# Kernel optimization log

Measured on AMD Instinct MI355X. Metric: run time of the kernel, lower is better.

The kernel has to match this reference:

```python
import jax, jax.numpy as jnp
import numpy as np

NUM_HEADS = 8
HEAD_DIM = 128
ATTN_SCALE = 0.12


def _rotary_tables(T, head_dim, dtype=jnp.float32):
    # modded-nanogpt half-truncated RoPE: rotate only first half of freq slots
    quarter = head_dim // 4
    angular = (1.0 / 1024.0) ** jnp.linspace(0.0, 1.0, quarter, dtype=dtype)
    angular = jnp.concatenate([angular, jnp.zeros(quarter, dtype=dtype)])  # [head_dim//2]
    t = jnp.arange(T, dtype=dtype)
    theta = t[:, None] * angular[None, :]  # [T, head_dim//2]
    return jnp.cos(theta), jnp.sin(theta)


def _apply_rotary(x, cos, sin):
    # x: [B, T, H, D]; cos/sin: [T, D//2]
    x1, x2 = jnp.split(x, 2, axis=-1)
    c = cos[None, :, None, :]
    s = sin[None, :, None, :]
    y1 = x1 * c + x2 * s
    y2 = -x1 * s + x2 * c
    return jnp.concatenate([y1, y2], axis=-1)


def _rms_norm(x):
    eps = jnp.asarray(jnp.finfo(x.dtype).eps, x.dtype)
    var = jnp.mean(jnp.square(x), axis=-1, keepdims=True)
    return x * jax.lax.rsqrt(var + eps)


def setup_inputs() -> dict:
    key = jax.random.key(0)
    k1, k2, k3, k4, k5 = jax.random.split(key, 5)
    B, T, D = 1, 4096, 1024
    hdim = NUM_HEADS * HEAD_DIM
    std = 0.5 * D ** (-0.5)
    x = jax.random.normal(k1, (B, T, D), dtype=jnp.float32)
    ve = jax.random.normal(k2, (B, T, hdim), dtype=jnp.float32)
    qkv_w = jax.random.normal(k3, (3, hdim, D), dtype=jnp.float32) * std
    lambdas = jnp.array([0.5, 0.5], dtype=jnp.float32)
    c_proj_w = jax.random.normal(k5, (D, hdim), dtype=jnp.float32) * std
    return {"x": x, "ve": ve, "qkv_w": qkv_w, "lambdas": lambdas, "c_proj_w": c_proj_w}


def reference(x, ve, qkv_w, lambdas, c_proj_w):
    B, T, D = x.shape
    H, Hd = NUM_HEADS, HEAD_DIM
    # QKV projection: qkv_w [3, H*Hd, D]
    qkv = jnp.einsum('btd,ckd->btck', x, qkv_w)  # [B, T, 3, H*Hd]
    qkv = qkv.reshape(B, T, 3, H, Hd)
    q, k, v = qkv[:, :, 0], qkv[:, :, 1], qkv[:, :, 2]  # [B, T, H, Hd]
    # QK RMSNorm
    q = _rms_norm(q)
    k = _rms_norm(k)
    # RoPE
    cos, sin = _rotary_tables(T, Hd, dtype=x.dtype)
    q = _apply_rotary(q, cos, sin)
    k = _apply_rotary(k, cos, sin)
    # value-embedding lambda mix
    v = lambdas[0] * v + lambdas[1] * ve.reshape(B, T, H, Hd)
    # causal attention with fixed scale 0.12 (block-causal FlexAttention mask)
    scores = jnp.einsum('bthd,bshd->bhts', q, k) * ATTN_SCALE  # [B, H, T, T]
    causal = jnp.tril(jnp.ones((T, T), dtype=bool))
    scores = jnp.where(causal[None, None], scores, jnp.asarray(-jnp.inf, scores.dtype))
    probs = jax.nn.softmax(scores, axis=-1)
    y = jnp.einsum('bhts,bshd->bthd', probs, v)  # [B, T, H, Hd]
    y = y.reshape(B, T, H * Hd)
    return y @ c_proj_w.T  # [B, T, D]
```

## Files before the change

kernel.cpp:

```cpp
#include <hip/hip_runtime.h>

typedef __bf16 bf16;
typedef __bf16 bf16x8 __attribute__((ext_vector_type(8)));
typedef __bf16 bf16x4 __attribute__((ext_vector_type(4)));
typedef __bf16 bf16x2 __attribute__((ext_vector_type(2)));
typedef float f32x4 __attribute__((ext_vector_type(4)));
typedef float f32x16 __attribute__((ext_vector_type(16)));
typedef int i32x4 __attribute__((ext_vector_type(4)));
typedef int i32x2 __attribute__((ext_vector_type(2)));

#define GLL16(gp, lp)                                                          \
  __builtin_amdgcn_global_load_lds(                                            \
      (const __attribute__((address_space(1))) unsigned int*)(gp),             \
      (__attribute__((address_space(3))) unsigned int*)(lp), 16, 0, 0)

__global__ __launch_bounds__(256) void cast3_f32_bf16(
    const float* __restrict__ a, bf16* __restrict__ oa, int na4,
    const float* __restrict__ b, bf16* __restrict__ ob, int nb4,
    const float* __restrict__ c, bf16* __restrict__ oc, int nc4) {
  int i = blockIdx.x * blockDim.x + threadIdx.x;
  int stride = gridDim.x * blockDim.x;
  int total = na4 + nb4 + nc4;
  for (; i < total; i += stride) {
    const float4* src;
    bf16x4* dst;
    int j = i;
    if (j < na4) {
      src = (const float4*)a + j; dst = (bf16x4*)oa + j;
    } else if ((j -= na4) < nb4) {
      src = (const float4*)b + j; dst = (bf16x4*)ob + j;
    } else {
      j -= nb4;
      src = (const float4*)c + j; dst = (bf16x4*)oc + j;
    }
    float4 v = *src;
    bf16x4 o;
    o[0] = (bf16)v.x; o[1] = (bf16)v.y; o[2] = (bf16)v.z; o[3] = (bf16)v.w;
    *dst = o;
  }
}

template <int K, int LDC, int BM, typename CT>
__global__ __launch_bounds__(256) void gemm_bt(
    const bf16* __restrict__ A, const bf16* __restrict__ B,
    CT* __restrict__ C) {
  __shared__ __align__(16) bf16 As[BM * 64];
  __shared__ __align__(16) bf16 Bs[128 * 64];
  const int tid  = threadIdx.x;
  const int lane = tid & 63;
  const int wave = tid >> 6;
  const int ln15 = lane & 15, quad = lane >> 4;
  const int wm = wave >> 1, wn = wave & 1;
  const int m0 = blockIdx.y * BM, n0 = blockIdx.x * 128;
  constexpr int MI = BM / 32;

  f32x4 acc[MI][4] = {};

  for (int k0 = 0; k0 < K; k0 += 64) {
    __syncthreads();
#pragma unroll
    for (int j = 0; j < BM / 32; ++j) {
      int gbase = j * 256 + wave * 64;
      int g = gbase + lane;
      int r = g >> 3, c = (g & 7) ^ (r & 7);
      GLL16(A + (size_t)(m0 + r) * K + k0 + c * 8, As + (size_t)gbase * 8);
    }
#pragma unroll
    for (int j = 0; j < 4; ++j) {
      int gbase = j * 256 + wave * 64;
      int g = gbase + lane;
      int r = g >> 3, c = (g & 7) ^ (r & 7);
      GLL16(B + (size_t)(n0 + r) * K + k0 + c * 8, Bs + (size_t)gbase * 8);
    }
    __syncthreads();
#pragma unroll
    for (int kk = 0; kk < 2; ++kk) {
      bf16x8 af[MI], bfr[4];
#pragma unroll
      for (int mi = 0; mi < MI; ++mi) {
        int m = wm * (BM / 2) + mi * 16 + ln15;
        int cg = kk * 4 + quad;
        af[mi] = *(const bf16x8*)(As + (m * 8 + (cg ^ (m & 7))) * 8);
      }
#pragma unroll
      for (int ni = 0; ni < 4; ++ni) {
        int n = wn * 64 + ni * 16 + ln15;
        int cg = kk * 4 + quad;
        bfr[ni] = *(const bf16x8*)(Bs + (n * 8 + (cg ^ (n & 7))) * 8);
      }
#pragma unroll
      for (int mi = 0; mi < MI; ++mi)
#pragma unroll
        for (int ni = 0; ni < 4; ++ni)
          acc[mi][ni] = __builtin_amdgcn_mfma_f32_16x16x32_bf16(
              af[mi], bfr[ni], acc[mi][ni], 0, 0, 0);
    }
  }
#pragma unroll
  for (int mi = 0; mi < MI; ++mi)
#pragma unroll
    for (int ni = 0; ni < 4; ++ni)
#pragma unroll
      for (int r = 0; r < 4; ++r) {
        int row = m0 + wm * (BM / 2) + mi * 16 + quad * 4 + r;
        int col = n0 + wn * 64 + ni * 16 + ln15;
        C[(size_t)row * LDC + col] = (CT)acc[mi][ni][r];
      }
}

__global__ __launch_bounds__(256) void qkv_post(
    const bf16* __restrict__ qkv, const float* __restrict__ ve,
    const float* __restrict__ lambdas, bf16* __restrict__ qn,
    bf16* __restrict__ kn, bf16* __restrict__ vt) {
  const int h  = blockIdx.x;
  const int t0 = blockIdx.y * 64;
  const int tid = threadIdx.x;
  const int wave = tid >> 6, lane = tid & 63;
  __shared__ __align__(16) float tile[64][129];

  const int j = lane;
  float cth = 1.0f, sth = 0.0f;
  for (int i = 0; i < 16; ++i) {
    int t = t0 + wave * 16 + i;
    if (j < 32) {
      float ang = exp2f((float)j * (-10.0f / 31.0f));
      float th = (float)t * ang;
      __sincosf(th, &sth, &cth);
    }
#pragma unroll
    for (int qk = 0; qk < 2; ++qk) {
      const bf16* row = qkv + (size_t)t * 3072 + qk * 1024 + h * 128;
      float x1 = (float)row[j], x2 = (float)row[j + 64];
      float ss = x1 * x1 + x2 * x2;
#pragma unroll
      for (int m = 1; m < 64; m <<= 1) ss += __shfl_xor(ss, m, 64);
      float rinv = rsqrtf(ss * (1.0f / 128.0f) + 1.1920929e-7f);
      if (qk == 0) rinv *= 0.12f;
      float y1 = (x1 * cth + x2 * sth) * rinv;
      float y2 = (x2 * cth - x1 * sth) * rinv;
      bf16* orow = (qk == 0 ? qn : kn) + (size_t)t * 1024 + h * 128;
      orow[j] = (bf16)y1;
      orow[j + 64] = (bf16)y2;
    }
  }

  float l0 = lambdas[0], l1 = lambdas[1];
  for (int c = 0; c < 32; ++c) {
    int idx = c * 256 + tid;
    int d = idx & 127, tl = idx >> 7;
    int t = t0 + tl;
    float v = (float)qkv[(size_t)t * 3072 + 2048 + h * 128 + d];
    float vev = ve[(size_t)t * 1024 + h * 128 + d];
    tile[tl][d] = l0 * v + l1 * vev;
  }
  __syncthreads();
  for (int c = 0; c < 32; ++c) {
    int idx = c * 256 + tid;
    int tl = idx & 63, d = idx >> 6;
    vt[((size_t)(h * 128 + d)) * 4096 + t0 + tl] = (bf16)tile[tl][d];
  }
}

__global__ __launch_bounds__(256, 2) void flash_attn(
    const bf16* __restrict__ qn, const bf16* __restrict__ kn,
    const bf16* __restrict__ vt, float* __restrict__ Op,
    float* __restrict__ ls) {
  const int id = blockIdx.x;
  const int qt = (id < 256) ? (31 - (id >> 4)) : ((id - 256) >> 4);
  const int sub = id & 15;
  const int h = sub >> 1;
  const int half = sub & 1;
  const int tid = threadIdx.x;
  const int wave = tid >> 6, lane = tid & 63;
  const int l31 = lane & 31, hl = lane >> 5;

  __shared__ __align__(16) bf16 smem[4 * 64 * 128];
  bf16* Ks = smem;
  bf16* Vs = smem + 2 * 64 * 128;

  const int nkv = 2 * (qt + 1);
  const int half0 = qt + 1;
  const int kt_begin = half ? half0 : 0;
  const int kt_end = half ? nkv : half0;
  const int niter = kt_end - kt_begin;
  const int pidx = (h * 32 + qt) * 2 + half;

  const int qminw = qt * 128 + wave * 32;
  const int qg = qminw + l31;

  bf16x8 qf[8];
  {
    const bf16* qb = qn + (size_t)qg * 1024 + h * 128 + hl * 8;
#pragma unroll
    for (int f = 0; f < 8; ++f) qf[f] = *(const bf16x8*)(qb + f * 16);
  }

  f32x16 acc_o[4] = {};
  float rs = 0.0f;

  auto prefetch = [&](int kt, int buf) {
    const int kv0 = kt * 64;
    bf16* ks = Ks + buf * (64 * 128);
    bf16* vs = Vs + buf * (128 * 64);
#pragma unroll
    for (int jj = 0; jj < 4; ++jj) {
      int gbase = jj * 256 + wave * 64;
      int g = gbase + lane;
      int r = g >> 4, c = (g & 15) ^ (r & 15);
      GLL16(kn + (size_t)(kv0 + r) * 1024 + h * 128 + c * 8,
            ks + (size_t)gbase * 8);
    }
#pragma unroll
    for (int jj = 0; jj < 4; ++jj) {
      int gbase = jj * 256 + wave * 64;
      int g = gbase + lane;
      int d = g >> 3, c = (g & 7) ^ (d & 7);
      GLL16(vt + ((size_t)(h * 128 + d)) * 4096 + kv0 + c * 8,
            vs + (size_t)gbase * 8);
    }
  };

  prefetch(kt_begin, 0);

  for (int it = 0; it < niter; ++it) {
    const int kt = kt_begin + it;
    const int kv0 = kt * 64;
    __syncthreads();
    if (it + 1 < niter) prefetch(kt + 1, (it + 1) & 1);
    const bf16* ksb = Ks + (it & 1) * (64 * 128);
    const bf16* vsb = Vs + (it & 1) * (128 * 64);

    if (kv0 > qminw + 31) continue;

    f32x16 acc0 = {}, acc1 = {};
    const int l15 = l31 & 15;
    __builtin_amdgcn_s_setprio(1);
#pragma unroll
    for (int f = 0; f < 8; ++f) {
      bf16x8 a0 = *(const bf16x8*)(
          ksb + (l31 * 16 + ((2 * f + hl) ^ l15)) * 8);
      bf16x8 a1 = *(const bf16x8*)(
          ksb + ((32 + l31) * 16 + ((2 * f + hl) ^ l15)) * 8);
      acc0 = __builtin_amdgcn_mfma_f32_32x32x16_bf16(a0, qf[f], acc0, 0, 0, 0);
      acc1 = __builtin_amdgcn_mfma_f32_32x32x16_bf16(a1, qf[f], acc1, 0, 0, 0);
    }
    __builtin_amdgcn_s_setprio(0);

    const bool needmask = (kv0 + 63 > qminw);
    float rsp[4] = {0.f, 0.f, 0.f, 0.f};
    if (needmask) {
#pragma unroll
      for (int r = 0; r < 16; ++r) {
        int kvl = (r & 3) + 8 * (r >> 2) + 4 * hl;
        float v0 = __expf(acc0[r]);
        float v1 = __expf(acc1[r]);
        if (kv0 + kvl > qg) v0 = 0.0f;
        if (kv0 + 32 + kvl > qg) v1 = 0.0f;
        acc0[r] = v0; acc1[r] = v1;
        rsp[r & 3] += v0 + v1;
      }
    } else {
#pragma unroll
      for (int r = 0; r < 16; ++r) {
        float v0 = __expf(acc0[r]);
        float v1 = __expf(acc1[r]);
        acc0[r] = v0; acc1[r] = v1;
        rsp[r & 3] += v0 + v1;
      }
    }
    rs += (rsp[0] + rsp[1]) + (rsp[2] + rsp[3]);

    int pk0[8], pk1[8];
#pragma unroll
    for (int g = 0; g < 8; ++g) {
      bf16x2 t0, t1;
      t0[0] = (bf16)acc0[2 * g]; t0[1] = (bf16)acc0[2 * g + 1];
      t1[0] = (bf16)acc1[2 * g]; t1[1] = (bf16)acc1[2 * g + 1];
      pk0[g] = __builtin_bit_cast(int, t0);
      pk1[g] = __builtin_bit_cast(int, t1);
    }

    bf16x8 pf[4];
#if __has_builtin(__builtin_amdgcn_permlane32_swap)
#pragma unroll
    for (int cc = 0; cc < 4; ++cc) {
      int s0 = (cc < 2) ? pk0[(cc & 1) * 4 + 0] : pk1[(cc & 1) * 4 + 0];
      int s1 = (cc < 2) ? pk0[(cc & 1) * 4 + 1] : pk1[(cc & 1) * 4 + 1];
      int s2 = (cc < 2) ? pk0[(cc & 1) * 4 + 2] : pk1[(cc & 1) * 4 + 2];
      int s3 = (cc < 2) ? pk0[(cc & 1) * 4 + 3] : pk1[(cc & 1) * 4 + 3];
      i32x2 r02 = __builtin_amdgcn_permlane32_swap(s0, s2, false, false);
      i32x2 r13 = __builtin_amdgcn_permlane32_swap(s1, s3, false, false);
      i32x4 dv;
      dv[0] = r02[0];
      dv[1] = r13[0];
      dv[2] = r02[1];
      dv[3] = r13[1];
      pf[cc] = __builtin_bit_cast(bf16x8, dv);
    }
#else
#pragma unroll
    for (int cc = 0; cc < 4; ++cc) {
      int s0 = (cc < 2) ? pk0[(cc & 1) * 4 + 0] : pk1[(cc & 1) * 4 + 0];
      int s1 = (cc < 2) ? pk0[(cc & 1) * 4 + 1] : pk1[(cc & 1) * 4 + 1];
      int s2 = (cc < 2) ? pk0[(cc & 1) * 4 + 2] : pk1[(cc & 1) * 4 + 2];
      int s3 = (cc < 2) ? pk0[(cc & 1) * 4 + 3] : pk1[(cc & 1) * 4 + 3];
      int sh0 = __shfl_xor(s0, 32, 64);
      int sh1 = __shfl_xor(s1, 32, 64);
      int sh2 = __shfl_xor(s2, 32, 64);
      int sh3 = __shfl_xor(s3, 32, 64);
      int own0 = hl ? s2 : s0;
      int own1 = hl ? s3 : s1;
      int par0 = hl ? sh2 : sh0;
      int par1 = hl ? sh3 : sh1;
      i32x4 dv;
      dv[0] = hl ? par0 : own0;
      dv[1] = hl ? par1 : own1;
      dv[2] = hl ? own0 : par0;
      dv[3] = hl ? own1 : par1;
      pf[cc] = __builtin_bit_cast(bf16x8, dv);
    }
#endif

    __builtin_amdgcn_s_setprio(1);
#pragma unroll
    for (int dt = 0; dt < 4; ++dt) {
      int vrow = dt * 32 + l31;
#pragma unroll
      for (int cc = 0; cc < 4; ++cc) {
        bf16x8 a = *(const bf16x8*)(
            vsb + (vrow * 8 + ((2 * cc + hl) ^ (vrow & 7))) * 8);
        acc_o[dt] =
            __builtin_amdgcn_mfma_f32_32x32x16_bf16(a, pf[cc], acc_o[dt], 0, 0, 0);
      }
    }
    __builtin_amdgcn_s_setprio(0);
  }

  rs += __shfl_xor(rs, 32, 64);
  if (hl == 0) ls[pidx * 128 + wave * 32 + l31] = rs;
  float* opb = Op + (size_t)pidx * 16384 + (size_t)(wave * 32 + l31) * 128;
#pragma unroll
  for (int dt = 0; dt < 4; ++dt)
#pragma unroll
    for (int rg = 0; rg < 4; ++rg) {
      float4 o;
      o.x = acc_o[dt][rg * 4 + 0];
      o.y = acc_o[dt][rg * 4 + 1];
      o.z = acc_o[dt][rg * 4 + 2];
      o.w = acc_o[dt][rg * 4 + 3];
      int d0 = dt * 32 + 4 * hl + 8 * rg;
      *(float4*)(opb + d0) = o;
    }
}

__global__ __launch_bounds__(256) void attn_combine(
    const float* __restrict__ Op, const float* __restrict__ ls,
    bf16* __restrict__ y) {
  int gid = blockIdx.x * 256 + threadIdx.x;
  int t = gid >> 8;
  int c4 = gid & 255;
  int qt = t >> 7, ql = t & 127;
  int h = c4 >> 5;
  int d = (c4 & 31) * 4;
  int pb = (h * 32 + qt) * 2;
  const float4 o0 = *(const float4*)(Op + (size_t)pb * 16384 + ql * 128 + d);
  const float4 o1 =
      *(const float4*)(Op + (size_t)(pb + 1) * 16384 + ql * 128 + d);
  float inv = 1.0f / (ls[pb * 128 + ql] + ls[(pb + 1) * 128 + ql]);
  bf16x4 o;
  o[0] = (bf16)((o0.x + o1.x) * inv);
  o[1] = (bf16)((o0.y + o1.y) * inv);
  o[2] = (bf16)((o0.z + o1.z) * inv);
  o[3] = (bf16)((o0.w + o1.w) * inv);
  *(bf16x4*)(y + (size_t)t * 1024 + h * 128 + d) = o;
}

extern "C" void kernel_launch(void* const* d_in, const int* in_sizes, int n_in,
                              void* d_out, int out_size, void* d_ws,
                              size_t ws_size, hipStream_t stream) {
  const float* x       = (const float*)d_in[0];
  const float* ve      = (const float*)d_in[1];
  const float* qkv_w   = (const float*)d_in[2];
  const float* lambdas = (const float*)d_in[3];
  const float* c_proj  = (const float*)d_in[4];
  float* out = (float*)d_out;

  char* ws = (char*)d_ws;
  bf16* qkv   = (bf16*)ws;
  bf16* xbf   = (bf16*)(ws + 25165824);
  bf16* wqkv  = (bf16*)(ws + 33554432);
  bf16* wproj = (bf16*)(ws + 39845888);
  bf16* qn    = (bf16*)(ws + 41943040);
  bf16* kn    = (bf16*)(ws + 50331648);
  bf16* vt    = (bf16*)(ws + 58720256);
  bf16* yb    = (bf16*)(ws + 67108864);
  float* Op  = (float*)ws;
  float* lsw = (float*)(ws + 33554432);

  cast3_f32_bf16<<<2048, 256, 0, stream>>>(x, xbf, 4194304 / 4, qkv_w, wqkv,
                                           3145728 / 4, c_proj, wproj,
                                           1048576 / 4);

  gemm_bt<1024, 3072, 128, bf16><<<dim3(24, 32), 256, 0, stream>>>(xbf, wqkv,
                                                                   qkv);

  qkv_post<<<dim3(8, 64), 256, 0, stream>>>(qkv, ve, lambdas, qn, kn, vt);

  flash_attn<<<512, 256, 0, stream>>>(qn, kn, vt, Op, lsw);
  attn_combine<<<4096, 256, 0, stream>>>(Op, lsw, yb);

  gemm_bt<1024, 1024, 64, float><<<dim3(8, 64), 256, 0, stream>>>(yb, wproj,
                                                                  out);
}
```

Before: 224.3 us.

## Balance flash-attention work with variable KV split-count per query tile

After: 236.5 us. +5.4%, slower.

```diff
diff --git a/kernel.cpp b/kernel.cpp
--- a/kernel.cpp
+++ b/kernel.cpp
@@ -166,10 +166,20 @@
     const bf16* __restrict__ vt, float* __restrict__ Op,
     float* __restrict__ ls) {
   const int id = blockIdx.x;
-  const int qt = (id < 256) ? (31 - (id >> 4)) : ((id - 256) >> 4);
-  const int sub = id & 15;
-  const int h = sub >> 1;
-  const int half = sub & 1;
+  const int h = id / 74;
+  const int r = 73 - (id % 74);
+  int qt, ch;
+  if (r < 9)       { qt = r;                 ch = 0; }
+  else if (r < 27) { qt = 9 + ((r - 9) >> 1);  ch = (r - 9) & 1; }
+  else if (r < 54) { qt = 18 + (r - 27) / 3;   ch = (r - 27) % 3; }
+  else             { qt = 27 + ((r - 54) >> 2); ch = (r - 54) & 3; }
+  const int nkv = 2 * (qt + 1);
+  const int nch = (nkv + 17) / 18;
+  const int cbase = nkv / nch, crem = nkv % nch;
+  const int kt_begin = ch * cbase + (ch < crem ? ch : crem);
+  const int niter = cbase + (ch < crem ? 1 : 0);
+  const int pidx = h * 74 + r;
+
   const int tid = threadIdx.x;
   const int wave = tid >> 6, lane = tid & 63;
   const int l31 = lane & 31, hl = lane >> 5;
@@ -177,13 +187,6 @@
   __shared__ __align__(16) bf16 smem[4 * 64 * 128];
   bf16* Ks = smem;
   bf16* Vs = smem + 2 * 64 * 128;
-
-  const int nkv = 2 * (qt + 1);
-  const int half0 = qt + 1;
-  const int kt_begin = half ? half0 : 0;
-  const int kt_end = half ? nkv : half0;
-  const int niter = kt_end - kt_begin;
-  const int pidx = (h * 32 + qt) * 2 + half;
 
   const int qminw = qt * 128 + wave * 32;
   const int qg = qminw + l31;
@@ -206,8 +209,8 @@
     for (int jj = 0; jj < 4; ++jj) {
       int gbase = jj * 256 + wave * 64;
       int g = gbase + lane;
-      int r = g >> 4, c = (g & 15) ^ (r & 15);
-      GLL16(kn + (size_t)(kv0 + r) * 1024 + h * 128 + c * 8,
+      int rr = g >> 4, c = (g & 15) ^ (rr & 15);
+      GLL16(kn + (size_t)(kv0 + rr) * 1024 + h * 128 + c * 8,
             ks + (size_t)gbase * 8);
     }
 #pragma unroll
@@ -250,22 +253,22 @@
     float rsp[4] = {0.f, 0.f, 0.f, 0.f};
     if (needmask) {
 #pragma unroll
-      for (int r = 0; r < 16; ++r) {
-        int kvl = (r & 3) + 8 * (r >> 2) + 4 * hl;
-        float v0 = __expf(acc0[r]);
-        float v1 = __expf(acc1[r]);
+      for (int rr = 0; rr < 16; ++rr) {
+        int kvl = (rr & 3) + 8 * (rr >> 2) + 4 * hl;
+        float v0 = __expf(acc0[rr]);
+        float v1 = __expf(acc1[rr]);
         if (kv0 + kvl > qg) v0 = 0.0f;
         if (kv0 + 32 + kvl > qg) v1 = 0.0f;
-        acc0[r] = v0; acc1[r] = v1;
-        rsp[r & 3] += v0 + v1;
+        acc0[rr] = v0; acc1[rr] = v1;
+        rsp[rr & 3] += v0 + v1;
       }
     } else {
 #pragma unroll
-      for (int r = 0; r < 16; ++r) {
-        float v0 = __expf(acc0[r]);
-        float v1 = __expf(acc1[r]);
-        acc0[r] = v0; acc1[r] = v1;
-        rsp[r & 3] += v0 + v1;
+      for (int rr = 0; rr < 16; ++rr) {
+        float v0 = __expf(acc0[rr]);
+        float v1 = __expf(acc1[rr]);
+        acc0[rr] = v0; acc1[rr] = v1;
+        rsp[rr & 3] += v0 + v1;
       }
     }
     rs += (rsp[0] + rsp[1]) + (rsp[2] + rsp[3]);
@@ -362,17 +365,26 @@
   int qt = t >> 7, ql = t & 127;
   int h = c4 >> 5;
   int d = (c4 & 31) * 4;
-  int pb = (h * 32 + qt) * 2;
-  const float4 o0 = *(const float4*)(Op + (size_t)pb * 16384 + ql * 128 + d);
-  const float4 o1 =
-      *(const float4*)(Op + (size_t)(pb + 1) * 16384 + ql * 128 + d);
-  float inv = 1.0f / (ls[pb * 128 + ql] + ls[(pb + 1) * 128 + ql]);
-  bf16x4 o;
-  o[0] = (bf16)((o0.x + o1.x) * inv);
-  o[1] = (bf16)((o0.y + o1.y) * inv);
-  o[2] = (bf16)((o0.z + o1.z) * inv);
-  o[3] = (bf16)((o0.w + o1.w) * inv);
-  *(bf16x4*)(y + (size_t)t * 1024 + h * 128 + d) = o;
+  int cs, nch;
+  if (qt < 9)       { cs = qt;               nch = 1; }
+  else if (qt < 18) { cs = 9 + 2 * (qt - 9);   nch = 2; }
+  else if (qt < 27) { cs = 27 + 3 * (qt - 18); nch = 3; }
+  else              { cs = 54 + 4 * (qt - 27); nch = 4; }
+  int pb = h * 74 + cs;
+  float4 o = {0.f, 0.f, 0.f, 0.f};
+  float l = 0.f;
+  for (int p = 0; p < nch; ++p) {
+    const float4 v = *(const float4*)(Op + (size_t)(pb + p) * 16384 + ql * 128 + d);
+    o.x += v.x; o.y += v.y; o.z += v.z; o.w += v.w;
+    l += ls[(pb + p) * 128 + ql];
+  }
+  float inv = 1.0f / l;
+  bf16x4 ov;
+  ov[0] = (bf16)(o.x * inv);
+  ov[1] = (bf16)(o.y * inv);
+  ov[2] = (bf16)(o.z * inv);
+  ov[3] = (bf16)(o.w * inv);
+  *(bf16x4*)(y + (size_t)t * 1024 + h * 128 + d) = ov;
 }
 
 extern "C" void kernel_launch(void* const* d_in, const int* in_sizes, int n_in,
@@ -395,7 +407,7 @@
   bf16* vt    = (bf16*)(ws + 58720256);
   bf16* yb    = (bf16*)(ws + 67108864);
   float* Op  = (float*)ws;
-  float* lsw = (float*)(ws + 33554432);
+  float* lsw = (float*)(ws + 38797312);
 
   cast3_f32_bf16<<<2048, 256, 0, stream>>>(x, xbf, 4194304 / 4, qkv_w, wqkv,
                                            3145728 / 4, c_proj, wproj,
@@ -406,7 +418,7 @@
 
   qkv_post<<<dim3(8, 64), 256, 0, stream>>>(qkv, ve, lambdas, qn, kn, vt);
 
-  flash_attn<<<512, 256, 0, stream>>>(qn, kn, vt, Op, lsw);
+  flash_attn<<<592, 256, 0, stream>>>(qn, kn, vt, Op, lsw);
   attn_combine<<<4096, 256, 0, stream>>>(Op, lsw, yb);
 
   gemm_bt<1024, 1024, 64, float><<<dim3(8, 64), 256, 0, stream>>>(yb, wproj,
```
